# Performance work log

Measured on AMD Instinct MI355X. Metric: run time of the kernel, lower is better.

The kernel has to match this reference:

```python
import jax, jax.numpy as jnp
import numpy as np
from jax import lax

NUM_HEADS = 8


def setup_inputs() -> dict:
    key = jax.random.key(0)
    k0, k1, k2, k3, k4 = jax.random.split(key, 5)
    B, N, C = 16, 4096, 256  # N = H*W = 64*64
    H = W = 64
    x = jax.random.normal(k0, (B, N, C), dtype=jnp.float32)
    w_qkv = jax.random.normal(k1, (3 * C, C), dtype=jnp.float32) * (1.0 / np.sqrt(C))
    w_proj = jax.random.normal(k2, (C, C), dtype=jnp.float32) * (1.0 / np.sqrt(C))
    b_proj = jax.random.normal(k3, (C,), dtype=jnp.float32) * 0.02
    conv_w = jax.random.normal(k4, (C, 1, 3, 3), dtype=jnp.float32) * (1.0 / 3.0)  # depthwise 3x3 for crpe
    return {"x": x, "w_qkv": w_qkv, "w_proj": w_proj, "b_proj": b_proj,
            "conv_w": conv_w, "H": H, "W": W}


def reference(x, w_qkv, w_proj, b_proj, conv_w, H, W):
    B, N, C = x.shape
    h = NUM_HEADS
    ch = C // h
    scale = ch ** (-0.5)

    # qkv projection -> (3, B, h, N, ch)
    qkv = (x @ w_qkv.T).reshape(B, N, 3, h, ch).transpose(2, 0, 3, 1, 4)
    q, k, v = qkv[0], qkv[1], qkv[2]

    # linear attention: softmax over keys (token dim), reassociated matmuls
    k_softmax = jax.nn.softmax(k, axis=2)                       # (B,h,N,ch)
    kv = jnp.einsum('bhnk,bhnv->bhkv', k_softmax, v)            # (B,h,ch,ch)
    factor_att = jnp.einsum('bhnk,bhkv->bhnv', q, kv)           # (B,h,N,ch)

    # crpe (semantic strength selector): q * depthwise_conv2d(v) on the HxW grid
    v_img = v.transpose(0, 1, 3, 2).reshape(B, h * ch, H, W)    # (B,C,H,W)
    conv_v = lax.conv_general_dilated(
        v_img, conv_w, window_strides=(1, 1), padding='SAME',
        feature_group_count=h * ch,
        dimension_numbers=('NCHW', 'OIHW', 'NCHW'))
    conv_v = conv_v.reshape(B, h, ch, N).transpose(0, 1, 3, 2)  # (B,h,N,ch)
    crpe = q * conv_v

    out = (scale * factor_att + crpe).transpose(0, 2, 1, 3).reshape(B, N, C)
    return out @ w_proj.T + b_proj
```

## Files before the change

### kernel.cpp

```cpp
#include <hip/hip_runtime.h>

typedef unsigned short u16;
typedef unsigned int   u32;
typedef __bf16 bf16x8 __attribute__((ext_vector_type(8)));
typedef float  f32x4  __attribute__((ext_vector_type(4)));

__device__ __forceinline__ float bf2f(u16 h){
  u32 u = ((u32)h) << 16;
  return __builtin_bit_cast(float, u);
}
__device__ __forceinline__ u16 f2bf(float f){
  u32 u = __builtin_bit_cast(u32, f);
  u32 lsb = (u >> 16) & 1u;
  u += 0x7fffu + lsb;
  return (u16)(u >> 16);
}
__device__ __forceinline__ float bflo(u32 u){ return __builtin_bit_cast(float, u << 16); }
__device__ __forceinline__ float bfhi(u32 u){ return __builtin_bit_cast(float, u & 0xffff0000u); }

#define AS3(p) ((__attribute__((address_space(3))) void*)(p))
#define AS1(p) ((const __attribute__((address_space(1))) void*)(p))

__global__ __launch_bounds__(256) void cvt_all(const float* __restrict__ x,  u16* __restrict__ xd,
                                               const float* __restrict__ wq, u16* __restrict__ wqd,
                                               const float* __restrict__ wp, u16* __restrict__ wpd){
  int blk = blockIdx.x;
  const float* s; u16* d; int i;
  if (blk < 8192){ s = x;  d = xd;  i = (blk * 256 + threadIdx.x) * 8; }
  else if (blk < 8288){ s = wq; d = wqd; i = ((blk - 8192) * 256 + threadIdx.x) * 8; }
  else { s = wp; d = wpd; i = ((blk - 8288) * 256 + threadIdx.x) * 8; }
  float4 a = *(const float4*)(s + i);
  float4 b = *(const float4*)(s + i + 4);
  u32 o0 = (u32)f2bf(a.x) | ((u32)f2bf(a.y) << 16);
  u32 o1 = (u32)f2bf(a.z) | ((u32)f2bf(a.w) << 16);
  u32 o2 = (u32)f2bf(b.x) | ((u32)f2bf(b.y) << 16);
  u32 o3 = (u32)f2bf(b.z) | ((u32)f2bf(b.w) << 16);
  *(uint4*)(d + i) = make_uint4(o0, o1, o2, o3);
}

__global__ __launch_bounds__(256) void gemm_qkv(
  const u16* __restrict__ A, const u16* __restrict__ Bm, char* __restrict__ outp)
{
  constexpr int K = 256;
  __shared__ __align__(16) char lds[65536];
  const int bid0 = blockIdx.x;
  const int bid = ((bid0 & 7) * 384) + (bid0 >> 3);
  const int tn = bid % 6, tm = bid / 6;
  const int m0 = tm * 128, n0 = tn * 128;
  const int tid  = threadIdx.x;
  const int lane = tid & 63, wid = tid >> 6;
  const int wm = (wid >> 1) * 64, wn = (wid & 1) * 64;
  const int l15 = lane & 15, l16 = lane >> 4;

  auto stage = [&](int buf, int kt){
    char* la = lds + buf * 32768;
    char* lb = la + 16384;
#pragma unroll
    for (int it = 0; it < 4; ++it){
      int ch  = it * 256 + tid;
      int row = ch >> 3;
      int k8  = (ch & 7) ^ (row & 7);
      __builtin_amdgcn_global_load_lds(AS1(A  + (size_t)(m0 + row) * K + kt * 64 + k8 * 8),
                                       AS3(la + ch * 16), 16, 0, 0);
      __builtin_amdgcn_global_load_lds(AS1(Bm + (size_t)(n0 + row) * K + kt * 64 + k8 * 8),
                                       AS3(lb + ch * 16), 16, 0, 0);
    }
  };

  f32x4 acc[4][4];
#pragma unroll
  for (int i = 0; i < 4; ++i)
#pragma unroll
    for (int j = 0; j < 4; ++j) acc[i][j] = (f32x4){0.f, 0.f, 0.f, 0.f};

  stage(0, 0);
  __syncthreads();
  constexpr int NT = K / 64;
  for (int kt = 0; kt < NT; ++kt){
    const int buf = kt & 1;
    if (kt + 1 < NT) stage(buf ^ 1, kt + 1);
    const char* la = lds + buf * 32768;
    const char* lb = la + 16384;
#pragma unroll
    for (int kk = 0; kk < 2; ++kk){
      bf16x8 af[4], bfr[4];
      const int ka = kk * 4 + l16;
#pragma unroll
      for (int f = 0; f < 4; ++f){
        int ra = wm + f * 16 + l15;
        af[f]  = *(const bf16x8*)(la + ra * 128 + (((ka ^ ra) & 7) << 4));
        int rb = wn + f * 16 + l15;
        bfr[f] = *(const bf16x8*)(lb + rb * 128 + (((ka ^ rb) & 7) << 4));
      }
#pragma unroll
      for (int fm = 0; fm < 4; ++fm)
#pragma unroll
        for (int fn = 0; fn < 4; ++fn)
          acc[fm][fn] = __builtin_amdgcn_mfma_f32_16x16x32_bf16(bfr[fn], af[fm], acc[fm][fn], 0, 0, 0);
    }
    __syncthreads();
  }

#pragma unroll
  for (int fm = 0; fm < 4; ++fm)
#pragma unroll
    for (int fn = 0; fn < 4; ++fn){
      int m = m0 + wm + fm * 16 + l15;
      int n = n0 + wn + fn * 16 + l16 * 4;
      u32 lo = (u32)f2bf(acc[fm][fn][0]) | ((u32)f2bf(acc[fm][fn][1]) << 16);
      u32 hi = (u32)f2bf(acc[fm][fn][2]) | ((u32)f2bf(acc[fm][fn][3]) << 16);
      int s = n >> 8, hd = (n >> 5) & 7, cc = n & 31;
      int bb = m >> 12, tok = m & 4095;
      u16* dst = (u16*)(outp + (size_t)s * 33554432u);
      *(uint2*)(dst + ((size_t)(bb * 8 + hd) * 4096 + tok) * 32 + cc) = make_uint2(lo, hi);
    }
}

__global__ __launch_bounds__(256) void kv_partial(const u16* __restrict__ Kb, const u16* __restrict__ Vb,
                                                  float* __restrict__ pkv, float* __restrict__ pden){
  __shared__ float E [64][32];
  __shared__ float Vf[64][32];
  const int bh = blockIdx.x >> 4, sp = blockIdx.x & 15;
  const int tid = threadIdx.x;
  const u16* kp = Kb + ((size_t)bh * 4096 + sp * 256) * 32;
  const u16* vp = Vb + ((size_t)bh * 4096 + sp * 256) * 32;
  const int c = tid & 31, g = tid >> 5;
  const int srow = tid >> 2, scol = (tid & 3) * 8;
  float a0 = 0.f, a1 = 0.f, a2 = 0.f, a3 = 0.f, den = 0.f;
  for (int chx = 0; chx < 4; ++chx){
    uint4 kb4 = *(const uint4*)(kp + chx * 2048 + tid * 8);
    uint4 vb4 = *(const uint4*)(vp + chx * 2048 + tid * 8);
    float4 e0, e1, v0, v1;
    e0.x = __expf(bflo(kb4.x)); e0.y = __expf(bfhi(kb4.x));
    e0.z = __expf(bflo(kb4.y)); e0.w = __expf(bfhi(kb4.y));
    e1.x = __expf(bflo(kb4.z)); e1.y = __expf(bfhi(kb4.z));
    e1.z = __expf(bflo(kb4.w)); e1.w = __expf(bfhi(kb4.w));
    v0.x = bflo(vb4.x); v0.y = bfhi(vb4.x);
    v0.z = bflo(vb4.y); v0.w = bfhi(vb4.y);
    v1.x = bflo(vb4.z); v1.y = bfhi(vb4.z);
    v1.z = bflo(vb4.w); v1.w = bfhi(vb4.w);
    *(float4*)&E [srow][scol]     = e0;  *(float4*)&E [srow][scol + 4] = e1;
    *(float4*)&Vf[srow][scol]     = v0;  *(float4*)&Vf[srow][scol + 4] = v1;
    __syncthreads();
#pragma unroll 4
    for (int nn = 0; nn < 64; ++nn){
      float e = E[nn][c];
      float4 vv = *(const float4*)&Vf[nn][g * 4];
      a0 += e * vv.x; a1 += e * vv.y; a2 += e * vv.z; a3 += e * vv.w;
      den += e;
    }
    __syncthreads();
  }
  size_t base = ((size_t)sp * 128 + bh) * 1024 + (size_t)c * 32 + g * 4;
  *(float4*)&pkv[base] = make_float4(a0, a1, a2, a3);
  if (g == 0) pden[((size_t)sp * 128 + bh) * 32 + c] = den;
}

__global__ __launch_bounds__(256) void kv_w2(const float* __restrict__ pkv, const float* __restrict__ pden,
                                             const float* __restrict__ wproj, u16* __restrict__ w2t){
  __shared__ float kv[1024];
  __shared__ float dn[32];
  const int bh = blockIdx.x, b = bh >> 3, hd = bh & 7;
  const int t = threadIdx.x;
  if (t < 32){
    float d = 0.f;
#pragma unroll
    for (int s = 0; s < 16; ++s) d += pden[((size_t)s * 128 + bh) * 32 + t];
    dn[t] = 0.17677669529663687f / d;
  }
  __syncthreads();
#pragma unroll
  for (int i = 0; i < 4; ++i){
    int idx = t + i * 256;
    float v = 0.f;
#pragma unroll
    for (int s = 0; s < 16; ++s) v += pkv[((size_t)s * 128 + bh) * 1024 + idx];
    kv[idx] = v * dn[idx >> 5];
  }
  __syncthreads();
  float wr[32];
  const float* wp = wproj + (size_t)t * 256 + hd * 32;
#pragma unroll
  for (int j = 0; j < 8; ++j){
    float4 w4 = ((const float4*)wp)[j];
    wr[j*4] = w4.x; wr[j*4+1] = w4.y; wr[j*4+2] = w4.z; wr[j*4+3] = w4.w;
  }
  u32 ou[16];
#pragma unroll
  for (int c = 0; c < 32; ++c){
    float acc = 0.f;
#pragma unroll
    for (int v4 = 0; v4 < 8; ++v4){
      float4 kk = *(const float4*)&kv[c * 32 + v4 * 4];
      acc += kk.x * wr[v4*4] + kk.y * wr[v4*4+1] + kk.z * wr[v4*4+2] + kk.w * wr[v4*4+3];
    }
    if (c & 1) ou[c >> 1] |= (u32)f2bf(acc) << 16; else ou[c >> 1] = f2bf(acc);
  }
  uint4* dst = (uint4*)(w2t + (size_t)b * 65536 + (size_t)t * 256 + hd * 32);
  dst[0] = make_uint4(ou[0],  ou[1],  ou[2],  ou[3]);
  dst[1] = make_uint4(ou[4],  ou[5],  ou[6],  ou[7]);
  dst[2] = make_uint4(ou[8],  ou[9],  ou[10], ou[11]);
  dst[3] = make_uint4(ou[12], ou[13], ou[14], ou[15]);
}

__global__ __launch_bounds__(256) void attn_crpe(const u16* __restrict__ Qb, const u16* __restrict__ Vb,
                                                 const float* __restrict__ cw, u16* __restrict__ tmp){
  __shared__ u16 VsB[6][66][32];
  const int bid = blockIdx.x;
  const int bh = bid >> 4, rbk = bid & 15;
  const int y0 = rbk * 4;
  const int tid = threadIdx.x;
  const int x = tid & 63, yi = tid >> 6;
  const int n = (y0 + yi) * 64 + x;

  for (int idx = tid; idx < 1584; idx += 256){
    int g8 = idx & 3, t2 = idx >> 2;
    int j  = t2 / 66, xc = t2 - j * 66;
    int gy = y0 - 1 + j, gx = xc - 1;
    uint4 v = make_uint4(0u, 0u, 0u, 0u);
    if ((unsigned)gy < 64u && (unsigned)gx < 64u)
      v = *(const uint4*)(Vb + ((size_t)bh * 4096 + gy * 64 + gx) * 32 + g8 * 8);
    *(uint4*)&VsB[j][xc][8 * (g8 ^ ((xc >> 1) & 3))] = v;
  }
  __syncthreads();

  float ca[32];
#pragma unroll
  for (int i = 0; i < 32; ++i) ca[i] = 0.f;
  const int hd = bh & 7;
  const float* wp = cw + hd * 288;
#pragma unroll
  for (int tap = 0; tap < 9; ++tap){
    const int j  = yi + tap / 3;
    const int xs = x + (tap % 3);
    const u16* vrow = &VsB[j][xs][0];
    const int swz = (xs >> 1) & 3;
#pragma unroll
    for (int g8 = 0; g8 < 4; ++g8){
      uint4 q4 = *(const uint4*)(vrow + 8 * (g8 ^ swz));
      const int c0 = g8 * 8;
      ca[c0+0] += wp[(c0+0)*9+tap] * bflo(q4.x);
      ca[c0+1] += wp[(c0+1)*9+tap] * bfhi(q4.x);
      ca[c0+2] += wp[(c0+2)*9+tap] * bflo(q4.y);
      ca[c0+3] += wp[(c0+3)*9+tap] * bfhi(q4.y);
      ca[c0+4] += wp[(c0+4)*9+tap] * bflo(q4.z);
      ca[c0+5] += wp[(c0+5)*9+tap] * bfhi(q4.z);
      ca[c0+6] += wp[(c0+6)*9+tap] * bflo(q4.w);
      ca[c0+7] += wp[(c0+7)*9+tap] * bfhi(q4.w);
    }
  }

  const u16* qrow = Qb + ((size_t)bh * 4096 + n) * 32;
  uint4 u0 = *(const uint4*)(qrow);
  uint4 u1 = *(const uint4*)(qrow + 8);
  uint4 u2 = *(const uint4*)(qrow + 16);
  uint4 u3 = *(const uint4*)(qrow + 24);
  float qf[32];
#define UQ(u, o) qf[o] = bflo(u); qf[(o)+1] = bfhi(u);
  UQ(u0.x, 0)  UQ(u0.y, 2)  UQ(u0.z, 4)  UQ(u0.w, 6)
  UQ(u1.x, 8)  UQ(u1.y, 10) UQ(u1.z, 12) UQ(u1.w, 14)
  UQ(u2.x, 16) UQ(u2.y, 18) UQ(u2.z, 20) UQ(u2.w, 22)
  UQ(u3.x, 24) UQ(u3.y, 26) UQ(u3.z, 28) UQ(u3.w, 30)
#undef UQ

  u32 ou[16];
#pragma unroll
  for (int p = 0; p < 16; ++p){
    float v0 = qf[2 * p]     * ca[2 * p];
    float v1 = qf[2 * p + 1] * ca[2 * p + 1];
    ou[p] = (u32)f2bf(v0) | ((u32)f2bf(v1) << 16);
  }
  uint4* dst = (uint4*)(tmp + ((size_t)bh * 4096 + n) * 32);
  dst[0] = make_uint4(ou[0],  ou[1],  ou[2],  ou[3]);
  dst[1] = make_uint4(ou[4],  ou[5],  ou[6],  ou[7]);
  dst[2] = make_uint4(ou[8],  ou[9],  ou[10], ou[11]);
  dst[3] = make_uint4(ou[12], ou[13], ou[14], ou[15]);
}

__global__ __launch_bounds__(256) void gemm_fin(
  const u16* __restrict__ Acr, const u16* __restrict__ Qb,
  const u16* __restrict__ Bw,  const u16* __restrict__ W2t,
  float* __restrict__ outp, const float* __restrict__ bias)
{
  __shared__ __align__(16) char lds[65536];
  const int bid0 = blockIdx.x;
  const int bid = ((bid0 & 7) * 128) + (bid0 >> 3);
  const int tn = bid & 1, tm = bid >> 1;
  const int m0 = tm * 128, n0 = tn * 128;
  const int b = m0 >> 12, nbase = m0 & 4095;
  const int tid  = threadIdx.x;
  const int lane = tid & 63, wid = tid >> 6;
  const int wm = (wid >> 1) * 64, wn = (wid & 1) * 64;
  const int l15 = lane & 15, l16 = lane >> 4;

  auto stage = [&](int buf, int kt){
    char* la = lds + buf * 32768;
    char* lb = la + 16384;
#pragma unroll
    for (int it = 0; it < 4; ++it){
      int ch  = it * 256 + tid;
      int row = ch >> 3;
      int k8  = (ch & 7) ^ (row & 7);
      int kp  = kt * 64 + k8 * 8;
      const u16* pl = (kp < 256) ? Acr : Qb;
      int kq = kp & 255, hd = kq >> 5, cc = kq & 31;
      const u16* asrc = pl + ((size_t)(b * 8 + hd) * 4096 + (nbase + row)) * 32 + cc;
      const u16* bsrc = (kp < 256)
        ? Bw  + (size_t)(n0 + row) * 256 + kp
        : W2t + (size_t)b * 65536 + (size_t)(n0 + row) * 256 + (kp - 256);
      __builtin_amdgcn_global_load_lds(AS1(asrc), AS3(la + ch * 16), 16, 0, 0);
      __builtin_amdgcn_global_load_lds(AS1(bsrc), AS3(lb + ch * 16), 16, 0, 0);
    }
  };

  f32x4 acc[4][4];
#pragma unroll
  for (int i = 0; i < 4; ++i)
#pragma unroll
    for (int j = 0; j < 4; ++j) acc[i][j] = (f32x4){0.f, 0.f, 0.f, 0.f};

  stage(0, 0);
  __syncthreads();
  constexpr int NT = 8;
  for (int kt = 0; kt < NT; ++kt){
    const int buf = kt & 1;
    if (kt + 1 < NT) stage(buf ^ 1, kt + 1);
    const char* la = lds + buf * 32768;
    const char* lb = la + 16384;
#pragma unroll
    for (int kk = 0; kk < 2; ++kk){
      bf16x8 af[4], bfr[4];
      const int ka = kk * 4 + l16;
#pragma unroll
      for (int f = 0; f < 4; ++f){
        int ra = wm + f * 16 + l15;
        af[f]  = *(const bf16x8*)(la + ra * 128 + (((ka ^ ra) & 7) << 4));
        int rb = wn + f * 16 + l15;
        bfr[f] = *(const bf16x8*)(lb + rb * 128 + (((ka ^ rb) & 7) << 4));
      }
#pragma unroll
      for (int fm = 0; fm < 4; ++fm)
#pragma unroll
        for (int fn = 0; fn < 4; ++fn)
          acc[fm][fn] = __builtin_amdgcn_mfma_f32_16x16x32_bf16(af[fm], bfr[fn], acc[fm][fn], 0, 0, 0);
    }
    __syncthreads();
  }

#pragma unroll
  for (int fm = 0; fm < 4; ++fm)
#pragma unroll
    for (int fn = 0; fn < 4; ++fn)
#pragma unroll
      for (int r = 0; r < 4; ++r){
        int m = m0 + wm + fm * 16 + l16 * 4 + r;
        int n = n0 + wn + fn * 16 + l15;
        outp[(size_t)m * 256 + n] = acc[fm][fn][r] + bias[n];
      }
}

extern "C" void kernel_launch(void* const* d_in, const int* in_sizes, int n_in,
                              void* d_out, int out_size, void* d_ws, size_t ws_size,
                              hipStream_t stream) {
  const float* x      = (const float*)d_in[0];
  const float* w_qkv  = (const float*)d_in[1];
  const float* w_proj = (const float*)d_in[2];
  const float* b_proj = (const float*)d_in[3];
  const float* conv_w = (const float*)d_in[4];

  char* ws = (char*)d_ws;
  char* ob = (char*)d_out;

  char*  qkvb   =          ws;
  u16*   Qb     = (u16*)  (ws);
  u16*   Kb     = (u16*)  (ws + 33554432);
  u16*   Vb     = (u16*)  (ws + 67108864);
  u16*   wprojb = (u16*)  (ws + 100663296);
  float* pkv    = (float*)(ws + 100794368);
  float* pden   = (float*)(ws + 109182976);
  u16*   w2t    = (u16*)  (ws + 109445120);

  u16*   xbf    = (u16*)  (ob);
  u16*   wqkvb  = (u16*)  (ob + 33554432);
  u16*   tmp    = Kb;

  cvt_all<<<8320, 256, 0, stream>>>(x, xbf, w_qkv, wqkvb, w_proj, wprojb);

  gemm_qkv<<<3072, 256, 0, stream>>>(xbf, wqkvb, qkvb);

  kv_partial<<<2048, 256, 0, stream>>>(Kb, Vb, pkv, pden);
  kv_w2<<<128, 256, 0, stream>>>(pkv, pden, w_proj, w2t);

  attn_crpe<<<2048, 256, 0, stream>>>(Qb, Vb, conv_w, tmp);

  gemm_fin<<<1024, 256, 0, stream>>>(tmp, Qb, wprojb, w2t, (float*)d_out, b_proj);
}
```

Before: 155.8 us.

## Fuse KV partial reduction with CRPE conv into one kernel sharing V tile

Merges the kv_partial and attn_crpe kernels into a single kv_crpe kernel. The V values for the kv accumulation are read from the halo-padded LDS tile already loaded for the depthwise conv, so V is read from global memory once instead of twice, and one kernel launch is removed. The CRPE result is packed into registers first and written to tmp, which aliases Kb, only after this block has finished reading its own K rows. The cost is higher register and LDS pressure per block, which may reduce occupancy.

```diff
diff --git a/kernel.cpp b/kernel.cpp
--- a/kernel.cpp
+++ b/kernel.cpp
@@ -116,99 +116,14 @@
     }
 }
 
-__global__ __launch_bounds__(256) void kv_partial(const u16* __restrict__ Kb, const u16* __restrict__ Vb,
-                                                  float* __restrict__ pkv, float* __restrict__ pden){
-  __shared__ float E [64][32];
-  __shared__ float Vf[64][32];
+__global__ __launch_bounds__(256) void kv_crpe(
+  const u16* __restrict__ Qb, const u16* __restrict__ Kb, const u16* __restrict__ Vb,
+  const float* __restrict__ cw, float* __restrict__ pkv, float* __restrict__ pden,
+  u16* __restrict__ tmp){
+  __shared__ u16 VsB[6][66][32];
+  __shared__ float E[64][32];
   const int bh = blockIdx.x >> 4, sp = blockIdx.x & 15;
-  const int tid = threadIdx.x;
-  const u16* kp = Kb + ((size_t)bh * 4096 + sp * 256) * 32;
-  const u16* vp = Vb + ((size_t)bh * 4096 + sp * 256) * 32;
-  const int c = tid & 31, g = tid >> 5;
-  const int srow = tid >> 2, scol = (tid & 3) * 8;
-  float a0 = 0.f, a1 = 0.f, a2 = 0.f, a3 = 0.f, den = 0.f;
-  for (int chx = 0; chx < 4; ++chx){
-    uint4 kb4 = *(const uint4*)(kp + chx * 2048 + tid * 8);
-    uint4 vb4 = *(const uint4*)(vp + chx * 2048 + tid * 8);
-    float4 e0, e1, v0, v1;
-    e0.x = __expf(bflo(kb4.x)); e0.y = __expf(bfhi(kb4.x));
-    e0.z = __expf(bflo(kb4.y)); e0.w = __expf(bfhi(kb4.y));
-    e1.x = __expf(bflo(kb4.z)); e1.y = __expf(bfhi(kb4.z));
-    e1.z = __expf(bflo(kb4.w)); e1.w = __expf(bfhi(kb4.w));
-    v0.x = bflo(vb4.x); v0.y = bfhi(vb4.x);
-    v0.z = bflo(vb4.y); v0.w = bfhi(vb4.y);
-    v1.x = bflo(vb4.z); v1.y = bfhi(vb4.z);
-    v1.z = bflo(vb4.w); v1.w = bfhi(vb4.w);
-    *(float4*)&E [srow][scol]     = e0;  *(float4*)&E [srow][scol + 4] = e1;
-    *(float4*)&Vf[srow][scol]     = v0;  *(float4*)&Vf[srow][scol + 4] = v1;
-    __syncthreads();
-#pragma unroll 4
-    for (int nn = 0; nn < 64; ++nn){
-      float e = E[nn][c];
-      float4 vv = *(const float4*)&Vf[nn][g * 4];
-      a0 += e * vv.x; a1 += e * vv.y; a2 += e * vv.z; a3 += e * vv.w;
-      den += e;
-    }
-    __syncthreads();
-  }
-  size_t base = ((size_t)sp * 128 + bh) * 1024 + (size_t)c * 32 + g * 4;
-  *(float4*)&pkv[base] = make_float4(a0, a1, a2, a3);
-  if (g == 0) pden[((size_t)sp * 128 + bh) * 32 + c] = den;
-}
-
-__global__ __launch_bounds__(256) void kv_w2(const float* __restrict__ pkv, const float* __restrict__ pden,
-                                             const float* __restrict__ wproj, u16* __restrict__ w2t){
-  __shared__ float kv[1024];
-  __shared__ float dn[32];
-  const int bh = blockIdx.x, b = bh >> 3, hd = bh & 7;
-  const int t = threadIdx.x;
-  if (t < 32){
-    float d = 0.f;
-#pragma unroll
-    for (int s = 0; s < 16; ++s) d += pden[((size_t)s * 128 + bh) * 32 + t];
-    dn[t] = 0.17677669529663687f / d;
-  }
-  __syncthreads();
-#pragma unroll
-  for (int i = 0; i < 4; ++i){
-    int idx = t + i * 256;
-    float v = 0.f;
-#pragma unroll
-    for (int s = 0; s < 16; ++s) v += pkv[((size_t)s * 128 + bh) * 1024 + idx];
-    kv[idx] = v * dn[idx >> 5];
-  }
-  __syncthreads();
-  float wr[32];
-  const float* wp = wproj + (size_t)t * 256 + hd * 32;
-#pragma unroll
-  for (int j = 0; j < 8; ++j){
-    float4 w4 = ((const float4*)wp)[j];
-    wr[j*4] = w4.x; wr[j*4+1] = w4.y; wr[j*4+2] = w4.z; wr[j*4+3] = w4.w;
-  }
-  u32 ou[16];
-#pragma unroll
-  for (int c = 0; c < 32; ++c){
-    float acc = 0.f;
-#pragma unroll
-    for (int v4 = 0; v4 < 8; ++v4){
-      float4 kk = *(const float4*)&kv[c * 32 + v4 * 4];
-      acc += kk.x * wr[v4*4] + kk.y * wr[v4*4+1] + kk.z * wr[v4*4+2] + kk.w * wr[v4*4+3];
-    }
-    if (c & 1) ou[c >> 1] |= (u32)f2bf(acc) << 16; else ou[c >> 1] = f2bf(acc);
-  }
-  uint4* dst = (uint4*)(w2t + (size_t)b * 65536 + (size_t)t * 256 + hd * 32);
-  dst[0] = make_uint4(ou[0],  ou[1],  ou[2],  ou[3]);
-  dst[1] = make_uint4(ou[4],  ou[5],  ou[6],  ou[7]);
-  dst[2] = make_uint4(ou[8],  ou[9],  ou[10], ou[11]);
-  dst[3] = make_uint4(ou[12], ou[13], ou[14], ou[15]);
-}
-
-__global__ __launch_bounds__(256) void attn_crpe(const u16* __restrict__ Qb, const u16* __restrict__ Vb,
-                                                 const float* __restrict__ cw, u16* __restrict__ tmp){
-  __shared__ u16 VsB[6][66][32];
-  const int bid = blockIdx.x;
-  const int bh = bid >> 4, rbk = bid & 15;
-  const int y0 = rbk * 4;
+  const int y0 = sp * 4;
   const int tid = threadIdx.x;
   const int x = tid & 63, yi = tid >> 6;
   const int n = (y0 + yi) * 64 + x;
@@ -249,28 +164,109 @@
       ca[c0+7] += wp[(c0+7)*9+tap] * bfhi(q4.w);
     }
   }
-
-  const u16* qrow = Qb + ((size_t)bh * 4096 + n) * 32;
-  uint4 u0 = *(const uint4*)(qrow);
-  uint4 u1 = *(const uint4*)(qrow + 8);
-  uint4 u2 = *(const uint4*)(qrow + 16);
-  uint4 u3 = *(const uint4*)(qrow + 24);
-  float qf[32];
+  u32 ou[16];
+  {
+    const u16* qrow = Qb + ((size_t)bh * 4096 + n) * 32;
+    uint4 u0 = *(const uint4*)(qrow);
+    uint4 u1 = *(const uint4*)(qrow + 8);
+    uint4 u2 = *(const uint4*)(qrow + 16);
+    uint4 u3 = *(const uint4*)(qrow + 24);
+    float qf[32];
 #define UQ(u, o) qf[o] = bflo(u); qf[(o)+1] = bfhi(u);
-  UQ(u0.x, 0)  UQ(u0.y, 2)  UQ(u0.z, 4)  UQ(u0.w, 6)
-  UQ(u1.x, 8)  UQ(u1.y, 10) UQ(u1.z, 12) UQ(u1.w, 14)
-  UQ(u2.x, 16) UQ(u2.y, 18) UQ(u2.z, 20) UQ(u2.w, 22)
-  UQ(u3.x, 24) UQ(u3.y, 26) UQ(u3.z, 28) UQ(u3.w, 30)
+    UQ(u0.x, 0)  UQ(u0.y, 2)  UQ(u0.z, 4)  UQ(u0.w, 6)
+    UQ(u1.x, 8)  UQ(u1.y, 10) UQ(u1.z, 12) UQ(u1.w, 14)
+    UQ(u2.x, 16) UQ(u2.y, 18) UQ(u2.z, 20) UQ(u2.w, 22)
+    UQ(u3.x, 24) UQ(u3.y, 26) UQ(u3.z, 28) UQ(u3.w, 30)
 #undef UQ
-
+#pragma unroll
+    for (int p = 0; p < 16; ++p){
+      float v0 = qf[2 * p]     * ca[2 * p];
+      float v1 = qf[2 * p + 1] * ca[2 * p + 1];
+      ou[p] = (u32)f2bf(v0) | ((u32)f2bf(v1) << 16);
+    }
+  }
+
+  const u16* kp = Kb + ((size_t)bh * 4096 + sp * 256) * 32;
+  const int c = tid & 31, g = tid >> 5;
+  const int srow = tid >> 2, scol = (tid & 3) * 8;
+  float a0 = 0.f, a1 = 0.f, a2 = 0.f, a3 = 0.f, den = 0.f;
+  for (int chx = 0; chx < 4; ++chx){
+    uint4 kb4 = *(const uint4*)(kp + chx * 2048 + tid * 8);
+    float4 e0, e1;
+    e0.x = __expf(bflo(kb4.x)); e0.y = __expf(bfhi(kb4.x));
+    e0.z = __expf(bflo(kb4.y)); e0.w = __expf(bfhi(kb4.y));
+    e1.x = __expf(bflo(kb4.z)); e1.y = __expf(bfhi(kb4.z));
+    e1.z = __expf(bflo(kb4.w)); e1.w = __expf(bfhi(kb4.w));
+    *(float4*)&E[srow][scol]     = e0;
+    *(float4*)&E[srow][scol + 4] = e1;
+    __syncthreads();
+    const int j = chx + 1;
+    const int goff = (g & 1) * 4;
+    const int G8 = g >> 1;
+#pragma unroll 4
+    for (int nn = 0; nn < 64; ++nn){
+      float e = E[nn][c];
+      int xc = nn + 1;
+      const u16* vp4 = &VsB[j][xc][8 * (G8 ^ ((xc >> 1) & 3)) + goff];
+      uint2 vv = *(const uint2*)vp4;
+      a0 += e * bflo(vv.x); a1 += e * bfhi(vv.x);
+      a2 += e * bflo(vv.y); a3 += e * bfhi(vv.y);
+      den += e;
+    }
+    __syncthreads();
+  }
+
+  size_t base = ((size_t)sp * 128 + bh) * 1024 + (size_t)c * 32 + g * 4;
+  *(float4*)&pkv[base] = make_float4(a0, a1, a2, a3);
+  if (g == 0) pden[((size_t)sp * 128 + bh) * 32 + c] = den;
+  uint4* dst = (uint4*)(tmp + ((size_t)bh * 4096 + n) * 32);
+  dst[0] = make_uint4(ou[0],  ou[1],  ou[2],  ou[3]);
+  dst[1] = make_uint4(ou[4],  ou[5],  ou[6],  ou[7]);
+  dst[2] = make_uint4(ou[8],  ou[9],  ou[10], ou[11]);
+  dst[3] = make_uint4(ou[12], ou[13], ou[14], ou[15]);
+}
+
+__global__ __launch_bounds__(256) void kv_w2(const float* __restrict__ pkv, const float* __restrict__ pden,
+                                             const float* __restrict__ wproj, u16* __restrict__ w2t){
+  __shared__ float kv[1024];
+  __shared__ float dn[32];
+  const int bh = blockIdx.x, b = bh >> 3, hd = bh & 7;
+  const int t = threadIdx.x;
+  if (t < 32){
+    float d = 0.f;
+#pragma unroll
+    for (int s = 0; s < 16; ++s) d += pden[((size_t)s * 128 + bh) * 32 + t];
+    dn[t] = 0.17677669529663687f / d;
+  }
+  __syncthreads();
+#pragma unroll
+  for (int i = 0; i < 4; ++i){
+    int idx = t + i * 256;
+    float v = 0.f;
+#pragma unroll
+    for (int s = 0; s < 16; ++s) v += pkv[((size_t)s * 128 + bh) * 1024 + idx];
+    kv[idx] = v * dn[idx >> 5];
+  }
+  __syncthreads();
+  float wr[32];
+  const float* wp = wproj + (size_t)t * 256 + hd * 32;
+#pragma unroll
+  for (int j = 0; j < 8; ++j){
+    float4 w4 = ((const float4*)wp)[j];
+    wr[j*4] = w4.x; wr[j*4+1] = w4.y; wr[j*4+2] = w4.z; wr[j*4+3] = w4.w;
+  }
   u32 ou[16];
 #pragma unroll
-  for (int p = 0; p < 16; ++p){
-    float v0 = qf[2 * p]     * ca[2 * p];
-    float v1 = qf[2 * p + 1] * ca[2 * p + 1];
-    ou[p] = (u32)f2bf(v0) | ((u32)f2bf(v1) << 16);
-  }
-  uint4* dst = (uint4*)(tmp + ((size_t)bh * 4096 + n) * 32);
+  for (int c = 0; c < 32; ++c){
+    float acc = 0.f;
+#pragma unroll
+    for (int v4 = 0; v4 < 8; ++v4){
+      float4 kk = *(const float4*)&kv[c * 32 + v4 * 4];
+      acc += kk.x * wr[v4*4] + kk.y * wr[v4*4+1] + kk.z * wr[v4*4+2] + kk.w * wr[v4*4+3];
+    }
+    if (c & 1) ou[c >> 1] |= (u32)f2bf(acc) << 16; else ou[c >> 1] = f2bf(acc);
+  }
+  uint4* dst = (uint4*)(w2t + (size_t)b * 65536 + (size_t)t * 256 + hd * 32);
   dst[0] = make_uint4(ou[0],  ou[1],  ou[2],  ou[3]);
   dst[1] = make_uint4(ou[4],  ou[5],  ou[6],  ou[7]);
   dst[2] = make_uint4(ou[8],  ou[9],  ou[10], ou[11]);
@@ -388,10 +384,8 @@
 
   gemm_qkv<<<3072, 256, 0, stream>>>(xbf, wqkvb, qkvb);
 
-  kv_partial<<<2048, 256, 0, stream>>>(Kb, Vb, pkv, pden);
+  kv_crpe<<<2048, 256, 0, stream>>>(Qb, Kb, Vb, conv_w, pkv, pden, tmp);
   kv_w2<<<128, 256, 0, stream>>>(pkv, pden, w_proj, w2t);
 
-  attn_crpe<<<2048, 256, 0, stream>>>(Qb, Vb, conv_w, tmp);
-
   gemm_fin<<<1024, 256, 0, stream>>>(tmp, Qb, wprojb, w2t, (float*)d_out, b_proj);
 }
```

Result: slower. 182.0 us (+16.8%).
